# Kernel tuning notes

Measured on AMD Instinct MI355X. Metric: run time of the kernel, lower is better.

The kernel has to match this reference:

```python
import jax, jax.numpy as jnp
import numpy as np

M, N, K = 35637, 15872, 20
FEAT = 128
EPS = 1e-5
W0 = 1.0  # Sine frequency


def setup_inputs() -> dict:
    key = jax.random.key(0)
    ks = jax.random.split(key, 8)
    x_feat = jax.random.normal(ks[0], (1, N, FEAT), dtype=jnp.float32)
    w_up_inputs = jax.random.uniform(ks[1], (1, 7, M, K), dtype=jnp.float32)
    idx = jax.random.randint(ks[2], (1, M, K), 0, N - 1)
    conv0_w = jax.random.normal(ks[3], (128, 7), dtype=jnp.float32) * (1.0 / np.sqrt(7))
    convs_w = jax.random.normal(ks[4], (7, 128, 128), dtype=jnp.float32) * (1.0 / np.sqrt(128))
    gammas = jnp.ones((8, 128), dtype=jnp.float32)
    betas = jnp.zeros((8, 128), dtype=jnp.float32)
    final_w = jax.random.normal(ks[5], (1, 128), dtype=jnp.float32) * (1.0 / np.sqrt(128))
    final_b = jnp.zeros((1,), dtype=jnp.float32)
    return {"x_feat": x_feat, "w_up_inputs": w_up_inputs, "idx": idx,
            "conv0_w": conv0_w, "convs_w": convs_w, "gammas": gammas,
            "betas": betas, "final_w": final_w, "final_b": final_b}


def _conv_bn_sine(h, W, g, b):
    # 1x1 conv == per-point matmul over channel dim; h: (B, M, K, Cin)
    h = jnp.einsum('bmkc,oc->bmko', h, W)
    # BatchNorm2d in training mode: batch stats over (B, M, K) per channel
    mu = jnp.mean(h, axis=(0, 1, 2))
    var = jnp.var(h, axis=(0, 1, 2))
    h = (h - mu) * jax.lax.rsqrt(var + EPS) * g + b
    return jnp.sin(W0 * h)


def reference(x_feat, w_up_inputs, idx, conv0_w, convs_w, gammas, betas, final_w, final_b):
    # w_up_inputs: (B, 7, M, K) -> channels-last (B, M, K, 7)
    h = jnp.transpose(w_up_inputs, (0, 2, 3, 1))
    h = _conv_bn_sine(h, conv0_w, gammas[0], betas[0])
    for i in range(7):
        h = _conv_bn_sine(h, convs_w[i], gammas[i + 1], betas[i + 1])
    # final 1x1 conv with bias -> logits (B, M, K, 1)
    logits = jnp.einsum('bmkc,oc->bmko', h, final_w) + final_b
    w = jax.nn.softmax(logits, axis=2)  # softmax over K neighbors
    # index_points: gather x_feat[b, idx[b, m, k], :] -> (B, M, K, FEAT)
    gathered = jax.vmap(lambda pts, ix: pts[ix])(x_feat, idx)
    feat_H = jnp.sum(w * gathered, axis=2)  # (B, M, FEAT)
    return feat_H
```

## Files before the change

kernel.cpp:

```cpp
#include <hip/hip_runtime.h>

#define PP 712740
#define MM 35637
#define KK 20
#define NF 15872
#define NTILES 44547
#define NSUPER 11137
#define ZROWS (NSUPER * 64)

typedef _Float16 h16;
typedef __attribute__((ext_vector_type(8))) _Float16 f16x8;
typedef __attribute__((ext_vector_type(4))) float f32x4;

__global__ __launch_bounds__(256) void k_zero(double* __restrict__ gs) {
  const int t = threadIdx.x;
#pragma unroll
  for (int i = 0; i < 8; ++i) gs[i * 256 + t] = 0.0;
}

__global__ __launch_bounds__(256) void k_layer0(
    const float* __restrict__ up,
    const float* __restrict__ w0,
    h16* __restrict__ z,
    double* __restrict__ gs)
{
  __shared__ float w0s[128 * 7];
  __shared__ h16 tb[4][2048];
  __shared__ double red[4][256];
  const int t = threadIdx.x;
  for (int i = t; i < 128 * 7; i += 256) w0s[i] = w0[i];
  __syncthreads();

  const int w = t >> 6;
  const int lane = t & 63;
  const int ln = lane & 15;
  const int q = lane >> 4;

  float sp[32], qp[32];
#pragma unroll
  for (int i = 0; i < 32; ++i) { sp[i] = 0.f; qp[i] = 0.f; }

  h16* tbw = &tb[w][0];

  const int gw = blockIdx.x * 4 + w;
  for (int tile = gw; tile < NTILES; tile += gridDim.x * 4) {
    const int p = tile * 16 + ln;
    const bool act = p < PP;
    float u[7];
#pragma unroll
    for (int c7 = 0; c7 < 7; ++c7) u[c7] = act ? up[c7 * PP + p] : 0.f;

#pragma unroll
    for (int ks = 0; ks < 4; ++ks) {
      f16x8 o;
#pragma unroll
      for (int j = 0; j < 8; ++j) {
        const int c = ks * 32 + q * 8 + j;
        float acc = 0.f;
#pragma unroll
        for (int c7 = 0; c7 < 7; ++c7) acc = fmaf(w0s[c * 7 + c7], u[c7], acc);
        if (!act) acc = 0.f;
        o[j] = (h16)acc;
        const int si = ks * 8 + j;
        sp[si] += acc;
        qp[si] = fmaf(acc, acc, qp[si]);
      }
      *(f16x8*)(tbw + ln * 128 + (((ks * 4 + q) ^ (ln & 7)) << 3)) = o;
    }

#pragma unroll
    for (int pass = 0; pass < 4; ++pass) {
      const int c = pass * 64 + lane;
      const int r = c >> 4;
      const int k = c & 15;
      const f16x8 v = *(const f16x8*)(tbw + r * 128 + ((k ^ (r & 7)) << 3));
      *(f16x8*)(z + (size_t)tile * 2048 + (size_t)c * 8) = v;
    }
  }

#pragma unroll
  for (int i = 0; i < 32; ++i) {
#pragma unroll
    for (int d = 1; d < 16; d <<= 1) {
      sp[i] += __shfl_xor(sp[i], d, 64);
      qp[i] += __shfl_xor(qp[i], d, 64);
    }
  }
  if (ln == 0) {
#pragma unroll
    for (int ks = 0; ks < 4; ++ks)
#pragma unroll
      for (int j = 0; j < 8; ++j) {
        const int c = ks * 32 + q * 8 + j;
        red[w][c] = (double)sp[ks * 8 + j];
        red[w][128 + c] = (double)qp[ks * 8 + j];
      }
  }
  __syncthreads();
  double v = red[0][t] + red[1][t] + red[2][t] + red[3][t];
  atomicAdd(&gs[t], v);
}

__global__ __launch_bounds__(256, 4) void k_layer(
    const h16* zin,
    h16* zout,
    const double* __restrict__ gsp,
    double* __restrict__ gso,
    const float* __restrict__ W,
    const float* __restrict__ gamma,
    const float* __restrict__ beta)
{
  __shared__ h16 actA[8192];
  __shared__ h16 actB[8192];
  __shared__ double red[256];

  const int t = threadIdx.x;
  const int w = t >> 6;
  const int lane = t & 63;
  const int ln = lane & 15;
  const int q = lane >> 4;
  const int G = (int)gridDim.x;

  float sc[8], sh[8];
  {
    const double n = (double)PP;
    const int cb = (t & 15) * 8;
#pragma unroll
    for (int j = 0; j < 8; ++j) {
      const int c = cb + j;
      const double mu = gsp[c] / n;
      const double var = gsp[128 + c] / n - mu * mu;
      const float rstd = (float)(1.0 / sqrt(var + 1e-5));
      sc[j] = rstd * gamma[c];
      sh[j] = beta[c] - (float)mu * sc[j];
    }
  }

  const int ob = w * 32;
  f16x8 wfr[2][4];
#pragma unroll
  for (int nt = 0; nt < 2; ++nt) {
    const int row_g = ob + (ln >> 2) * 8 + nt * 4 + (ln & 3);
    const float* wrow = W + (size_t)row_g * 128;
#pragma unroll
    for (int ks = 0; ks < 4; ++ks) {
      const float* src = wrow + ks * 32 + q * 8;
      const float4 aa = *(const float4*)src;
      const float4 bb = *(const float4*)(src + 4);
      f16x8 b;
      b[0] = (h16)aa.x; b[1] = (h16)aa.y; b[2] = (h16)aa.z; b[3] = (h16)aa.w;
      b[4] = (h16)bb.x; b[5] = (h16)bb.y; b[6] = (h16)bb.z; b[7] = (h16)bb.w;
      wfr[nt][ks] = b;
    }
  }

  float sp[8], qp[8];
#pragma unroll
  for (int i = 0; i < 8; ++i) { sp[i] = 0.f; qp[i] = 0.f; }

  const size_t roff = (size_t)(t >> 4) * 128 + (size_t)(t & 15) * 8;
  const int wbase = (t >> 4) * 256 + (((t & 15) ^ ((t >> 4) & 7)) << 4);
  int raddr[4];
#pragma unroll
  for (int ks = 0; ks < 4; ++ks)
    raddr[ks] = ln * 256 + (((ks * 4 + q) ^ (ln & 7)) << 4);
  const int obase = ln * 256 + (((w * 4 + q) ^ (ln & 7)) << 4);
  const int rbase = (t >> 4) * 256 + (((t & 15) ^ ((t >> 4) & 7)) << 4);

  int stile = blockIdx.x;
  f16x8 raw[4];
  {
    const h16* src = zin + (size_t)stile * 8192 + roff;
#pragma unroll
    for (int s = 0; s < 4; ++s) raw[s] = *(const f16x8*)(src + s * 2048);
  }

  char* A = (char*)actA;
  char* B = (char*)actB;

  for (; stile < NSUPER; stile += G) {
#pragma unroll
    for (int s = 0; s < 4; ++s) {
      f16x8 av;
#pragma unroll
      for (int j = 0; j < 8; ++j)
        av[j] = (h16)__sinf(fmaf((float)raw[s][j], sc[j], sh[j]));
      *(f16x8*)(A + (wbase + s * 4096)) = av;
    }

    {
      const int nxt = (stile + G < NSUPER) ? stile + G : NSUPER - 1;
      const h16* src = zin + (size_t)nxt * 8192 + roff;
#pragma unroll
      for (int s = 0; s < 4; ++s) raw[s] = *(const f16x8*)(src + s * 2048);
    }

    asm volatile("s_waitcnt lgkmcnt(0)\n\ts_barrier" ::: "memory");

#pragma unroll
    for (int ot = 0; ot < 4; ++ot) {
      f16x8 afr[4];
#pragma unroll
      for (int ks = 0; ks < 4; ++ks)
        afr[ks] = *(const f16x8*)(A + (ot * 4096 + raddr[ks]));

      f32x4 acc0 = (f32x4){0.f, 0.f, 0.f, 0.f};
      f32x4 acc1 = (f32x4){0.f, 0.f, 0.f, 0.f};
#pragma unroll
      for (int ks = 0; ks < 4; ++ks) {
        acc0 = __builtin_amdgcn_mfma_f32_16x16x32_f16(wfr[0][ks], afr[ks], acc0, 0, 0, 0);
        acc1 = __builtin_amdgcn_mfma_f32_16x16x32_f16(wfr[1][ks], afr[ks], acc1, 0, 0, 0);
      }

      const int p = stile * 64 + ot * 16 + ln;
      if (p < PP) {
#pragma unroll
        for (int r = 0; r < 4; ++r) {
          sp[r]     += acc0[r];
          qp[r]      = fmaf(acc0[r], acc0[r], qp[r]);
          sp[4 + r] += acc1[r];
          qp[4 + r]  = fmaf(acc1[r], acc1[r], qp[4 + r]);
        }
      }
      f16x8 o;
      o[0] = (h16)acc0[0]; o[1] = (h16)acc0[1]; o[2] = (h16)acc0[2]; o[3] = (h16)acc0[3];
      o[4] = (h16)acc1[0]; o[5] = (h16)acc1[1]; o[6] = (h16)acc1[2]; o[7] = (h16)acc1[3];
      *(f16x8*)(B + (ot * 4096 + obase)) = o;
    }

    asm volatile("s_waitcnt lgkmcnt(0)\n\ts_barrier" ::: "memory");

    {
      const size_t zo = (size_t)stile * 8192;
#pragma unroll
      for (int pass = 0; pass < 4; ++pass) {
        const f16x8 v = *(const f16x8*)(B + (pass * 4096 + rbase));
        *(f16x8*)(zout + zo + (size_t)pass * 2048 + (size_t)t * 8) = v;
      }
    }
  }

#pragma unroll
  for (int i = 0; i < 8; ++i) {
#pragma unroll
    for (int d = 1; d < 16; d <<= 1) {
      sp[i] += __shfl_xor(sp[i], d, 64);
      qp[i] += __shfl_xor(qp[i], d, 64);
    }
  }
  if (ln == 0) {
#pragma unroll
    for (int r = 0; r < 4; ++r) {
      const int c = ob + q * 8 + r;
      red[c]           = (double)sp[r];
      red[c + 4]       = (double)sp[4 + r];
      red[128 + c]     = (double)qp[r];
      red[128 + c + 4] = (double)qp[4 + r];
    }
  }
  __syncthreads();
  atomicAdd(&gso[t], red[t]);
}

__global__ __launch_bounds__(256) void k_outf(
    const h16* __restrict__ z,
    const double* __restrict__ gsp,
    const float* __restrict__ gamma,
    const float* __restrict__ beta,
    const float* __restrict__ fw,
    const float* __restrict__ fb,
    const int* __restrict__ idx,
    const float* __restrict__ xf,
    float* __restrict__ out)
{
  const int gw = (int)((blockIdx.x * 256 + threadIdx.x) >> 6);
  const int lane = (int)(threadIdx.x & 63);
  if (gw >= MM) return;
  const int m = gw;
  const int c0 = lane * 2;

  float scv[2], shv[2], fv[2];
#pragma unroll
  for (int j = 0; j < 2; ++j) {
    const int c = c0 + j;
    const double n = (double)PP;
    const double mu = gsp[c] / n;
    const double var = gsp[128 + c] / n - mu * mu;
    const float rstd = (float)(1.0 / sqrt(var + 1e-5));
    scv[j] = rstd * gamma[c];
    shv[j] = beta[c] - (float)mu * scv[j];
    fv[j] = fw[c];
  }
  const float fbv = fb[0];

  float l[KK];
#pragma unroll
  for (int k = 0; k < KK; ++k) {
    const h16* zp = z + (size_t)(m * KK + k) * 128 + c0;
    float part = fv[0] * __sinf(fmaf((float)zp[0], scv[0], shv[0]))
               + fv[1] * __sinf(fmaf((float)zp[1], scv[1], shv[1]));
#pragma unroll
    for (int d = 1; d < 64; d <<= 1) part += __shfl_xor(part, d, 64);
    l[k] = part + fbv;
  }

  float mx = l[0];
#pragma unroll
  for (int k = 1; k < KK; ++k) mx = fmaxf(mx, l[k]);
  float ssum = 0.f;
#pragma unroll
  for (int k = 0; k < KK; ++k) { l[k] = __expf(l[k] - mx); ssum += l[k]; }
  const float inv = 1.f / ssum;

  float a0 = 0.f, a1 = 0.f;
#pragma unroll
  for (int k = 0; k < KK; ++k) {
    const int r = idx[m * KK + k];
    const float wk = l[k] * inv;
    a0 = fmaf(wk, xf[r * 128 + lane], a0);
    a1 = fmaf(wk, xf[r * 128 + 64 + lane], a1);
  }
  out[m * 128 + lane] = a0;
  out[m * 128 + 64 + lane] = a1;
}

__global__ __launch_bounds__(256) void k_out(
    const float* __restrict__ logits,
    const int* __restrict__ idx,
    const float* __restrict__ xf,
    float* __restrict__ out)
{
  const int gw = (int)((blockIdx.x * 256 + threadIdx.x) >> 6);
  const int lane = threadIdx.x & 63;
  if (gw >= MM) return;
  const int m = gw;

  float l[KK];
#pragma unroll
  for (int k = 0; k < KK; ++k) l[k] = logits[m * KK + k];
  float mx = l[0];
#pragma unroll
  for (int k = 1; k < KK; ++k) mx = fmaxf(mx, l[k]);
  float ssum = 0.f;
#pragma unroll
  for (int k = 0; k < KK; ++k) { l[k] = __expf(l[k] - mx); ssum += l[k]; }
  const float inv = 1.f / ssum;

  float a0 = 0.f, a1 = 0.f;
#pragma unroll
  for (int k = 0; k < KK; ++k) {
    const int r = idx[m * KK + k];
    const float wk = l[k] * inv;
    a0 = fmaf(wk, xf[r * 128 + lane], a0);
    a1 = fmaf(wk, xf[r * 128 + 64 + lane], a1);
  }
  out[m * 128 + lane] = a0;
  out[m * 128 + 64 + lane] = a1;
}

__global__ __launch_bounds__(256) void k_chain(
    const float* __restrict__ up,
    const float* __restrict__ w0,
    const float* __restrict__ wc,
    const float* __restrict__ gam,
    const float* __restrict__ bet,
    const double* __restrict__ gs,
    double* __restrict__ gso,
    int jl, int mode,
    const float* __restrict__ fw,
    const float* __restrict__ fb,
    float* __restrict__ logits)
{
  __shared__ float sc_s[8][128], sh_s[8][128];
  __shared__ double bred[4][256];
  const int t = threadIdx.x;
  const int lane = t & 63;

  const int nbn = (mode == 0) ? jl : 8;
  for (int i = t; i < nbn * 128; i += 256) {
    const int L = i >> 7, c = i & 127;
    const double n = (double)PP;
    const double mu = gs[L * 256 + c] / n;
    const double var = gs[L * 256 + 128 + c] / n - mu * mu;
    const float rstd = (float)(1.0 / sqrt(var + 1e-5));
    const float sc = rstd * gam[L * 128 + c];
    sc_s[L][c] = sc;
    sh_s[L][c] = bet[L * 128 + c] - (float)mu * sc;
  }
  __syncthreads();

  double lS0 = 0, lS1 = 0, lQ0 = 0, lQ1 = 0;

  for (int p0 = blockIdx.x * 256; p0 < PP; p0 += gridDim.x * 256) {
    const int p = p0 + t;
    const bool act = p < PP;

    float a[128];
    {
      float u[7];
#pragma unroll
      for (int c = 0; c < 7; ++c) u[c] = act ? up[c * PP + p] : 0.f;
#pragma unroll 1
      for (int och = 0; och < 16; ++och) {
#pragma unroll
        for (int j = 0; j < 8; ++j) {
          float acc = 0.f;
#pragma unroll
          for (int c = 0; c < 7; ++c)
            acc = fmaf(w0[(och * 8 + j) * 7 + c], u[c], acc);
          a[och * 8 + j] = acc;
        }
      }
    }

#pragma unroll 1
    for (int L = 0; L < jl; ++L) {
#pragma unroll
      for (int c = 0; c < 128; ++c)
        a[c] = act ? __sinf(fmaf(a[c], sc_s[L][c], sh_s[L][c])) : 0.f;
      float b[128];
      const float* W = wc + (size_t)L * 128 * 128;
#pragma unroll 1
      for (int och = 0; och < 16; ++och) {
#pragma unroll
        for (int j = 0; j < 8; ++j) {
          float acc = 0.f;
#pragma unroll
          for (int c = 0; c < 128; ++c)
            acc = fmaf(W[(och * 8 + j) * 128 + c], a[c], acc);
          b[och * 8 + j] = acc;
        }
      }
#pragma unroll
      for (int c = 0; c < 128; ++c) a[c] = b[c];
    }

    if (mode == 0) {
#pragma unroll
      for (int o = 0; o < 128; ++o) {
        float s = a[o];
        float qv = a[o] * a[o];
#pragma unroll
        for (int d = 32; d > 0; d >>= 1) {
          s += __shfl_xor(s, d, 64);
          qv += __shfl_xor(qv, d, 64);
        }
        if ((o & 63) == lane) {
          if (o < 64) { lS0 += (double)s; lQ0 += (double)qv; }
          else        { lS1 += (double)s; lQ1 += (double)qv; }
        }
      }
    } else if (act) {
      float acc = fb[0];
#pragma unroll
      for (int c = 0; c < 128; ++c) {
        const float h = fmaf(a[c], sc_s[7][c], sh_s[7][c]);
        acc = fmaf(fw[c], __sinf(h), acc);
      }
      logits[p] = acc;
    }
  }

  if (mode == 0) {
    const int w = t >> 6;
    bred[w][lane]       = lS0;
    bred[w][64 + lane]  = lS1;
    bred[w][128 + lane] = lQ0;
    bred[w][192 + lane] = lQ1;
    __syncthreads();
    double v = bred[0][t] + bred[1][t] + bred[2][t] + bred[3][t];
    atomicAdd(&gso[t], v);
  }
}

extern "C" void kernel_launch(void* const* d_in, const int* in_sizes, int n_in,
                              void* d_out, int out_size, void* d_ws, size_t ws_size,
                              hipStream_t stream) {
  const float* xf  = (const float*)d_in[0];
  const float* up  = (const float*)d_in[1];
  const int*   idx = (const int*)d_in[2];
  const float* w0  = (const float*)d_in[3];
  const float* wc  = (const float*)d_in[4];
  const float* gam = (const float*)d_in[5];
  const float* bet = (const float*)d_in[6];
  const float* fw  = (const float*)d_in[7];
  const float* fb  = (const float*)d_in[8];
  float* out = (float*)d_out;

  char* ws = (char*)d_ws;
  const size_t zb     = (size_t)ZROWS * 128 * sizeof(h16);
  const size_t statsb = 8 * 256 * sizeof(double);
  const int NB = 1024;
  const int nbo = (MM + 3) / 4;

  if (ws_size >= 2 * zb + statsb) {
    h16* z0 = (h16*)ws;
    h16* z1 = (h16*)(ws + zb);
    double* gs = (double*)(ws + 2 * zb);

    k_zero<<<1, 256, 0, stream>>>(gs);
    k_layer0<<<NB, 256, 0, stream>>>(up, w0, z0, gs);
    h16* cur = z0;
    for (int i = 1; i <= 7; ++i) {
      h16* nxt = (i & 1) ? z1 : z0;
      k_layer<<<NB, 256, 0, stream>>>(cur, nxt,
                                      gs + (size_t)(i - 1) * 256,
                                      gs + (size_t)i * 256,
                                      wc + (size_t)(i - 1) * 128 * 128,
                                      gam + (size_t)(i - 1) * 128,
                                      bet + (size_t)(i - 1) * 128);
      cur = nxt;
    }
    k_outf<<<nbo, 256, 0, stream>>>(cur, gs + 7 * 256, gam + 7 * 128,
                                    bet + 7 * 128, fw, fb, idx, xf, out);
  } else if (ws_size >= zb + statsb) {
    h16* z = (h16*)ws;
    double* gs = (double*)(ws + zb);

    k_zero<<<1, 256, 0, stream>>>(gs);
    k_layer0<<<NB, 256, 0, stream>>>(up, w0, z, gs);
    for (int i = 1; i <= 7; ++i) {
      k_layer<<<NB, 256, 0, stream>>>(z, z,
                                      gs + (size_t)(i - 1) * 256,
                                      gs + (size_t)i * 256,
                                      wc + (size_t)(i - 1) * 128 * 128,
                                      gam + (size_t)(i - 1) * 128,
                                      bet + (size_t)(i - 1) * 128);
    }
    k_outf<<<nbo, 256, 0, stream>>>(z, gs + 7 * 256, gam + 7 * 128,
                                    bet + 7 * 128, fw, fb, idx, xf, out);
  } else {
    double* gs = (double*)ws;
    float* logits = (float*)(ws + statsb);

    k_zero<<<1, 256, 0, stream>>>(gs);
    for (int j = 0; j <= 7; ++j) {
      k_chain<<<NB, 256, 0, stream>>>(up, w0, wc, gam, bet, gs,
                                      gs + (size_t)j * 256, j, 0,
                                      fw, fb, logits);
    }
    k_chain<<<NB, 256, 0, stream>>>(up, w0, wc, gam, bet, gs,
                                    nullptr, 7, 1, fw, fb, logits);
    k_out<<<nbo, 256, 0, stream>>>(logits, idx, xf, out);
  }
}
```

Before: 713.7 us.

## Recompute layer-0 conv inside fused layer-1 kernel instead of storing it

Layer 0 no longer writes its fp16 activation tensor. A stats-only pass computes the batch statistics, and a new fused kernel recomputes the 7-to-128 conv from the raw inputs, applies BN and sine, and runs the layer-1 MFMA matmul. This removes one full write and read of the roughly 180MB intermediate, at the cost of reading the 7-channel input twice and doing extra FMAs. The output kernel also switches to vectorized 8-wide fp16 loads, with four neighbors handled per wavefront in parallel.

```diff
diff --git a/kernel.cpp b/kernel.cpp
--- a/kernel.cpp
+++ b/kernel.cpp
@@ -18,17 +18,15 @@
   for (int i = 0; i < 8; ++i) gs[i * 256 + t] = 0.0;
 }
 
-__global__ __launch_bounds__(256) void k_layer0(
+__global__ __launch_bounds__(256) void k_stats0(
     const float* __restrict__ up,
     const float* __restrict__ w0,
-    h16* __restrict__ z,
     double* __restrict__ gs)
 {
   __shared__ float w0s[128 * 7];
-  __shared__ h16 tb[4][2048];
   __shared__ double red[4][256];
   const int t = threadIdx.x;
-  for (int i = t; i < 128 * 7; i += 256) w0s[i] = w0[i];
+  for (int i = t; i < 128 * 7; i += 256) w0s[i] = (float)(h16)w0[i];
   __syncthreads();
 
   const int w = t >> 6;
@@ -39,8 +37,6 @@
   float sp[32], qp[32];
 #pragma unroll
   for (int i = 0; i < 32; ++i) { sp[i] = 0.f; qp[i] = 0.f; }
-
-  h16* tbw = &tb[w][0];
 
   const int gw = blockIdx.x * 4 + w;
   for (int tile = gw; tile < NTILES; tile += gridDim.x * 4) {
@@ -48,34 +44,20 @@
     const bool act = p < PP;
     float u[7];
 #pragma unroll
-    for (int c7 = 0; c7 < 7; ++c7) u[c7] = act ? up[c7 * PP + p] : 0.f;
-
-#pragma unroll
-    for (int ks = 0; ks < 4; ++ks) {
-      f16x8 o;
+    for (int c7 = 0; c7 < 7; ++c7) u[c7] = act ? up[(size_t)c7 * PP + p] : 0.f;
+
+#pragma unroll
+    for (int ks = 0; ks < 4; ++ks)
 #pragma unroll
       for (int j = 0; j < 8; ++j) {
         const int c = ks * 32 + q * 8 + j;
         float acc = 0.f;
 #pragma unroll
         for (int c7 = 0; c7 < 7; ++c7) acc = fmaf(w0s[c * 7 + c7], u[c7], acc);
-        if (!act) acc = 0.f;
-        o[j] = (h16)acc;
         const int si = ks * 8 + j;
         sp[si] += acc;
         qp[si] = fmaf(acc, acc, qp[si]);
       }
-      *(f16x8*)(tbw + ln * 128 + (((ks * 4 + q) ^ (ln & 7)) << 3)) = o;
-    }
-
-#pragma unroll
-    for (int pass = 0; pass < 4; ++pass) {
-      const int c = pass * 64 + lane;
-      const int r = c >> 4;
-      const int k = c & 15;
-      const f16x8 v = *(const f16x8*)(tbw + r * 128 + ((k ^ (r & 7)) << 3));
-      *(f16x8*)(z + (size_t)tile * 2048 + (size_t)c * 8) = v;
-    }
   }
 
 #pragma unroll
@@ -99,6 +81,177 @@
   __syncthreads();
   double v = red[0][t] + red[1][t] + red[2][t] + red[3][t];
   atomicAdd(&gs[t], v);
+}
+
+__global__ __launch_bounds__(256, 3) void k_layer1(
+    const float* __restrict__ up,
+    const float* __restrict__ w0,
+    h16* __restrict__ zout,
+    const double* __restrict__ gsp,
+    double* __restrict__ gso,
+    const float* __restrict__ W,
+    const float* __restrict__ gamma,
+    const float* __restrict__ beta)
+{
+  __shared__ h16 actA[8192];
+  __shared__ h16 actB[8192];
+  __shared__ double red[256];
+
+  const int t = threadIdx.x;
+  const int w = t >> 6;
+  const int lane = t & 63;
+  const int ln = lane & 15;
+  const int q = lane >> 4;
+  const int G = (int)gridDim.x;
+
+  float sc[8], sh[8];
+  {
+    const double n = (double)PP;
+    const int cb = (t & 15) * 8;
+#pragma unroll
+    for (int j = 0; j < 8; ++j) {
+      const int c = cb + j;
+      const double mu = gsp[c] / n;
+      const double var = gsp[128 + c] / n - mu * mu;
+      const float rstd = (float)(1.0 / sqrt(var + 1e-5));
+      sc[j] = rstd * gamma[c];
+      sh[j] = beta[c] - (float)mu * sc[j];
+    }
+  }
+
+  h16 w0h[7][8];
+  {
+    const int cb = (t & 15) * 8;
+#pragma unroll
+    for (int c7 = 0; c7 < 7; ++c7)
+#pragma unroll
+      for (int j = 0; j < 8; ++j)
+        w0h[c7][j] = (h16)w0[(cb + j) * 7 + c7];
+  }
+
+  const int ob = w * 32;
+  f16x8 wfr[2][4];
+#pragma unroll
+  for (int nt = 0; nt < 2; ++nt) {
+    const int row_g = ob + (ln >> 2) * 8 + nt * 4 + (ln & 3);
+    const float* wrow = W + (size_t)row_g * 128;
+#pragma unroll
+    for (int ks = 0; ks < 4; ++ks) {
+      const float* src = wrow + ks * 32 + q * 8;
+      const float4 aa = *(const float4*)src;
+      const float4 bb = *(const float4*)(src + 4);
+      f16x8 b;
+      b[0] = (h16)aa.x; b[1] = (h16)aa.y; b[2] = (h16)aa.z; b[3] = (h16)aa.w;
+      b[4] = (h16)bb.x; b[5] = (h16)bb.y; b[6] = (h16)bb.z; b[7] = (h16)bb.w;
+      wfr[nt][ks] = b;
+    }
+  }
+
+  float sp[8], qp[8];
+#pragma unroll
+  for (int i = 0; i < 8; ++i) { sp[i] = 0.f; qp[i] = 0.f; }
+
+  const int wbase = (t >> 4) * 256 + (((t & 15) ^ ((t >> 4) & 7)) << 4);
+  int raddr[4];
+#pragma unroll
+  for (int ks = 0; ks < 4; ++ks)
+    raddr[ks] = ln * 256 + (((ks * 4 + q) ^ (ln & 7)) << 4);
+  const int obase = ln * 256 + (((w * 4 + q) ^ (ln & 7)) << 4);
+  const int rbase = (t >> 4) * 256 + (((t & 15) ^ ((t >> 4) & 7)) << 4);
+
+  char* A = (char*)actA;
+  char* B = (char*)actB;
+
+  for (int stile = blockIdx.x; stile < NSUPER; stile += G) {
+    float u[4][7];
+#pragma unroll
+    for (int s = 0; s < 4; ++s) {
+      const int p = stile * 64 + (t >> 4) + 16 * s;
+      const bool act = p < PP;
+#pragma unroll
+      for (int c7 = 0; c7 < 7; ++c7)
+        u[s][c7] = act ? up[(size_t)c7 * PP + p] : 0.f;
+    }
+
+#pragma unroll
+    for (int s = 0; s < 4; ++s) {
+      f16x8 av;
+#pragma unroll
+      for (int j = 0; j < 8; ++j) {
+        float acc = 0.f;
+#pragma unroll
+        for (int c7 = 0; c7 < 7; ++c7)
+          acc = fmaf((float)w0h[c7][j], u[s][c7], acc);
+        av[j] = (h16)__sinf(fmaf(acc, sc[j], sh[j]));
+      }
+      *(f16x8*)(A + (wbase + s * 4096)) = av;
+    }
+
+    asm volatile("s_waitcnt lgkmcnt(0)\n\ts_barrier" ::: "memory");
+
+#pragma unroll
+    for (int ot = 0; ot < 4; ++ot) {
+      f16x8 afr[4];
+#pragma unroll
+      for (int ks = 0; ks < 4; ++ks)
+        afr[ks] = *(const f16x8*)(A + (ot * 4096 + raddr[ks]));
+
+      f32x4 acc0 = (f32x4){0.f, 0.f, 0.f, 0.f};
+      f32x4 acc1 = (f32x4){0.f, 0.f, 0.f, 0.f};
+#pragma unroll
+      for (int ks = 0; ks < 4; ++ks) {
+        acc0 = __builtin_amdgcn_mfma_f32_16x16x32_f16(wfr[0][ks], afr[ks], acc0, 0, 0, 0);
+        acc1 = __builtin_amdgcn_mfma_f32_16x16x32_f16(wfr[1][ks], afr[ks], acc1, 0, 0, 0);
+      }
+
+      const int p = stile * 64 + ot * 16 + ln;
+      if (p < PP) {
+#pragma unroll
+        for (int r = 0; r < 4; ++r) {
+          sp[r]     += acc0[r];
+          qp[r]      = fmaf(acc0[r], acc0[r], qp[r]);
+          sp[4 + r] += acc1[r];
+          qp[4 + r]  = fmaf(acc1[r], acc1[r], qp[4 + r]);
+        }
+      }
+      f16x8 o;
+      o[0] = (h16)acc0[0]; o[1] = (h16)acc0[1]; o[2] = (h16)acc0[2]; o[3] = (h16)acc0[3];
+      o[4] = (h16)acc1[0]; o[5] = (h16)acc1[1]; o[6] = (h16)acc1[2]; o[7] = (h16)acc1[3];
+      *(f16x8*)(B + (ot * 4096 + obase)) = o;
+    }
+
+    asm volatile("s_waitcnt lgkmcnt(0)\n\ts_barrier" ::: "memory");
+
+    {
+      const size_t zo = (size_t)stile * 8192;
+#pragma unroll
+      for (int pass = 0; pass < 4; ++pass) {
+        const f16x8 v = *(const f16x8*)(B + (pass * 4096 + rbase));
+        *(f16x8*)(zout + zo + (size_t)pass * 2048 + (size_t)t * 8) = v;
+      }
+    }
+  }
+
+#pragma unroll
+  for (int i = 0; i < 8; ++i) {
+#pragma unroll
+    for (int d = 1; d < 16; d <<= 1) {
+      sp[i] += __shfl_xor(sp[i], d, 64);
+      qp[i] += __shfl_xor(qp[i], d, 64);
+    }
+  }
+  if (ln == 0) {
+#pragma unroll
+    for (int r = 0; r < 4; ++r) {
+      const int c = ob + q * 8 + r;
+      red[c]           = (double)sp[r];
+      red[c + 4]       = (double)sp[4 + r];
+      red[128 + c]     = (double)qp[r];
+      red[128 + c + 4] = (double)qp[4 + r];
+    }
+  }
+  __syncthreads();
+  atomicAdd(&gso[t], red[t]);
 }
 
 __global__ __launch_bounds__(256, 4) void k_layer(
@@ -277,11 +430,13 @@
   const int lane = (int)(threadIdx.x & 63);
   if (gw >= MM) return;
   const int m = gw;
-  const int c0 = lane * 2;
-
-  float scv[2], shv[2], fv[2];
-#pragma unroll
-  for (int j = 0; j < 2; ++j) {
+  const int ln = lane & 15;
+  const int q = lane >> 4;
+  const int c0 = ln * 8;
+
+  float scv[8], shv[8], fv[8];
+#pragma unroll
+  for (int j = 0; j < 8; ++j) {
     const int c = c0 + j;
     const double n = (double)PP;
     const double mu = gsp[c] / n;
@@ -293,32 +448,59 @@
   }
   const float fbv = fb[0];
 
-  float l[KK];
-#pragma unroll
-  for (int k = 0; k < KK; ++k) {
-    const h16* zp = z + (size_t)(m * KK + k) * 128 + c0;
-    float part = fv[0] * __sinf(fmaf((float)zp[0], scv[0], shv[0]))
-               + fv[1] * __sinf(fmaf((float)zp[1], scv[1], shv[1]));
-#pragma unroll
-    for (int d = 1; d < 64; d <<= 1) part += __shfl_xor(part, d, 64);
-    l[k] = part + fbv;
-  }
-
-  float mx = l[0];
-#pragma unroll
-  for (int k = 1; k < KK; ++k) mx = fmaxf(mx, l[k]);
+  float lg[5];
+#pragma unroll
+  for (int g = 0; g < 5; ++g) {
+    const h16* zp = z + (size_t)(m * KK + g * 4 + q) * 128 + c0;
+    const f16x8 raw = *(const f16x8*)zp;
+    float part = 0.f;
+#pragma unroll
+    for (int j = 0; j < 8; ++j)
+      part = fmaf(fv[j], __sinf(fmaf((float)raw[j], scv[j], shv[j])), part);
+    part += __shfl_xor(part, 1, 64);
+    part += __shfl_xor(part, 2, 64);
+    part += __shfl_xor(part, 4, 64);
+    part += __shfl_xor(part, 8, 64);
+    lg[g] = part + fbv;
+  }
+
+  float l1[5], l2[5], l3[5];
+#pragma unroll
+  for (int g = 0; g < 5; ++g) {
+    l1[g] = __shfl_xor(lg[g], 16, 64);
+    l2[g] = __shfl_xor(lg[g], 32, 64);
+    l3[g] = __shfl_xor(l1[g], 32, 64);
+  }
+
+  float mx = lg[0];
+#pragma unroll
+  for (int g = 0; g < 5; ++g) {
+    mx = fmaxf(mx, lg[g]); mx = fmaxf(mx, l1[g]);
+    mx = fmaxf(mx, l2[g]); mx = fmaxf(mx, l3[g]);
+  }
+  float w0e[5], w1e[5], w2e[5], w3e[5];
   float ssum = 0.f;
 #pragma unroll
-  for (int k = 0; k < KK; ++k) { l[k] = __expf(l[k] - mx); ssum += l[k]; }
+  for (int g = 0; g < 5; ++g) {
+    w0e[g] = __expf(lg[g] - mx); ssum += w0e[g];
+    w1e[g] = __expf(l1[g] - mx); ssum += w1e[g];
+    w2e[g] = __expf(l2[g] - mx); ssum += w2e[g];
+    w3e[g] = __expf(l3[g] - mx); ssum += w3e[g];
+  }
   const float inv = 1.f / ssum;
 
   float a0 = 0.f, a1 = 0.f;
 #pragma unroll
-  for (int k = 0; k < KK; ++k) {
-    const int r = idx[m * KK + k];
-    const float wk = l[k] * inv;
-    a0 = fmaf(wk, xf[r * 128 + lane], a0);
-    a1 = fmaf(wk, xf[r * 128 + 64 + lane], a1);
+  for (int g = 0; g < 5; ++g) {
+#pragma unroll
+    for (int e = 0; e < 4; ++e) {
+      const int k = 4 * g + (q ^ e);
+      const float we = (e == 0 ? w0e[g] : e == 1 ? w1e[g] : e == 2 ? w2e[g] : w3e[g]);
+      const int r = idx[m * KK + k];
+      const float wk = we * inv;
+      a0 = fmaf(wk, xf[r * 128 + lane], a0);
+      a1 = fmaf(wk, xf[r * 128 + 64 + lane], a1);
+    }
   }
   out[m * 128 + lane] = a0;
   out[m * 128 + 64 + lane] = a1;
@@ -499,10 +681,12 @@
     double* gs = (double*)(ws + 2 * zb);
 
     k_zero<<<1, 256, 0, stream>>>(gs);
-    k_layer0<<<NB, 256, 0, stream>>>(up, w0, z0, gs);
+    k_stats0<<<NB, 256, 0, stream>>>(up, w0, gs);
+    k_layer1<<<NB, 256, 0, stream>>>(up, w0, z0, gs, gs + 256,
+                                     wc, gam, bet);
     h16* cur = z0;
-    for (int i = 1; i <= 7; ++i) {
-      h16* nxt = (i & 1) ? z1 : z0;
+    for (int i = 2; i <= 7; ++i) {
+      h16* nxt = (cur == z0) ? z1 : z0;
       k_layer<<<NB, 256, 0, stream>>>(cur, nxt,
                                       gs + (size_t)(i - 1) * 256,
                                       gs + (size_t)i * 256,
@@ -518,8 +702,10 @@
     double* gs = (double*)(ws + zb);
 
     k_zero<<<1, 256, 0, stream>>>(gs);
-    k_layer0<<<NB, 256, 0, stream>>>(up, w0, z, gs);
-    for (int i = 1; i <= 7; ++i) {
+    k_stats0<<<NB, 256, 0, stream>>>(up, w0, gs);
+    k_layer1<<<NB, 256, 0, stream>>>(up, w0, z, gs, gs + 256,
+                                     wc, gam, bet);
+    for (int i = 2; i <= 7; ++i) {
       k_layer<<<NB, 256, 0, stream>>>(z, z,
                                       gs + (size_t)(i - 1) * 256,
                                       gs + (size_t)i * 256,
```

Measured after the change: 704.4 us (median of 2 runs). No clear change (-1.3%).
